# Kernel optimization log

Hardware: AMD Instinct MI355X
Metric: run time of the kernel (lower is better)

The kernel has to match this reference:

```python
import jax, jax.numpy as jnp
import numpy as np


def _relative_position_index(S):
    # Faithful to the torch buffer construction, computed once with numpy (static).
    coords = np.stack(np.meshgrid(np.arange(S), np.arange(S), indexing='ij'))  # (2,S,S)
    coords = coords.reshape(2, -1)                                             # (2,N)
    rel = coords[:, :, None] - coords[:, None, :]                              # (2,N,N)
    rel = rel.transpose(1, 2, 0).astype(np.int64)                              # (N,N,2)
    rel[:, :, 0] += S - 1
    rel[:, :, 1] += S - 1
    rel[:, :, 0] *= 2 * S - 1
    idx = rel.sum(-1)
    idx = idx[::-1, ::-1].copy()  # flipud(fliplr(...))
    return idx                    # (N,N) int64 in [0, (2S-1)^2)


def setup_inputs() -> dict:
    key = jax.random.key(0)
    ks = jax.random.split(key, 6)
    B, S, C, NH = 8, 32, 512, 16
    x = jax.random.normal(ks[0], (B, S, S, C), dtype=jnp.float32)
    qkv_w = jax.random.normal(ks[1], (3 * C, C), dtype=jnp.float32) * 0.02
    qkv_b = jax.random.normal(ks[2], (3 * C,), dtype=jnp.float32) * 0.02
    rpb = jax.random.normal(ks[3], (NH, 2 * S - 1, 2 * S - 1), dtype=jnp.float32) * 0.02
    proj_w = jax.random.normal(ks[4], (C, C), dtype=jnp.float32) * 0.02
    proj_b = jax.random.normal(ks[5], (C,), dtype=jnp.float32) * 0.02
    return {"x": x, "qkv_w": qkv_w, "qkv_b": qkv_b, "rpb": rpb,
            "proj_w": proj_w, "proj_b": proj_b}


def reference(x, qkv_w, qkv_b, rpb, proj_w, proj_b):
    B, H, W, C = x.shape
    N = H * W
    num_heads = rpb.shape[0]
    head_dim = C // num_heads
    scale = head_dim ** (-0.5)
    S = H

    idx = _relative_position_index(S)  # static numpy (N,N)

    qkv = x.reshape(B, N, C) @ qkv_w.T + qkv_b            # (B,N,3C)
    qkv = qkv.reshape(B, N, 3, num_heads, head_dim)
    qkv = jnp.transpose(qkv, (2, 0, 3, 1, 4))             # (3,B,h,N,d)
    q, k, v = qkv[0], qkv[1], qkv[2]

    attn = jnp.einsum('bhnd,bhmd->bhnm', q * scale, k)    # (B,h,N,N)
    # gather relative position bias: (h,(2S-1)^2)[:, idx] -> (h,N,N)
    bias = rpb.reshape(num_heads, -1)[:, idx]
    attn = jax.nn.softmax(attn + bias[None], axis=-1)

    out = jnp.einsum('bhnm,bhmd->bhnd', attn, v)          # (B,h,N,d)
    out = jnp.transpose(out, (0, 2, 1, 3)).reshape(B, H, W, C)
    return out @ proj_w.T + proj_b
```

## Files before the change

### kernel.cpp

```cpp
#include <hip/hip_runtime.h>

typedef __bf16 bf16x8 __attribute__((ext_vector_type(8)));
typedef float f32x4 __attribute__((ext_vector_type(4)));
typedef unsigned int u32x2 __attribute__((ext_vector_type(2)));
typedef unsigned short u16;
typedef unsigned int u32;

__device__ __forceinline__ float bf2f(u16 v) {
    union { unsigned u; float f; } x; x.u = ((unsigned)v) << 16; return x.f;
}
__device__ __forceinline__ u16 f2bf(float f) {
    union { float f; unsigned u; } x; x.f = f;
    unsigned r = x.u + 0x7fffu + ((x.u >> 16) & 1u);
    return (u16)(r >> 16);
}

__device__ __forceinline__ bool probe_is_f32(const void* xp) {
    const unsigned* p = (const unsigned*)xp;
    int hits = 0;
#pragma unroll
    for (int i = 0; i < 32; i++) {
        const unsigned e = (p[i] >> 7) & 0xffu;
        hits += (e >= 0x90u) ? 1 : 0;
    }
    return hits > 3;
}

__device__ __forceinline__ float ld1(const void* p, size_t i, bool isf32) {
    return isf32 ? ((const float*)p)[i] : bf2f(((const u16*)p)[i]);
}

__device__ __forceinline__ void gl2lds16(const void* g, void* l) {
    __builtin_amdgcn_global_load_lds(
        (const __attribute__((address_space(1))) u32*)g,
        (__attribute__((address_space(3))) u32*)l, 16, 0, 0);
}

__global__ __launch_bounds__(256)
void convert_inputs(const void* __restrict__ x, const void* __restrict__ qw,
                    const void* __restrict__ qb, const void* __restrict__ pw,
                    const void* __restrict__ pb, const void* __restrict__ rp,
                    u16* __restrict__ xbf, u16* __restrict__ qwbf,
                    u16* __restrict__ qbbf, u16* __restrict__ pwbf,
                    u16* __restrict__ pbbf, float* __restrict__ rpl2e)
{
    const bool isf32 = probe_is_f32(x);
    const int gid = blockIdx.x * 256 + threadIdx.x;
    const int gsz = gridDim.x * 256;

    struct Seg { const void* s; u16* d; int n; };
    const Seg segs[5] = {{x, xbf, 4194304}, {qw, qwbf, 786432}, {pw, pwbf, 262144},
                         {qb, qbbf, 1536}, {pb, pbbf, 512}};
    for (int t = 0; t < 5; t++) {
        const int n4 = segs[t].n >> 2;
        if (isf32) {
            const f32x4* s = (const f32x4*)segs[t].s;
            for (int i = gid; i < n4; i += gsz) {
                f32x4 v = s[i];
                ushort4 o;
                o.x = f2bf(v[0]); o.y = f2bf(v[1]); o.z = f2bf(v[2]); o.w = f2bf(v[3]);
                *(ushort4*)(segs[t].d + i * 4) = o;
            }
        } else {
            const ushort4* s = (const ushort4*)segs[t].s;
            for (int i = gid; i < n4; i += gsz) *(ushort4*)(segs[t].d + i * 4) = s[i];
        }
    }
    for (int i = gid; i < 63504; i += gsz)
        rpl2e[i] = ld1(rp, i, isf32) * 1.4426950408889634f;
}

template<int MODE, int BM>
__global__ __launch_bounds__(256, MODE == 1 ? 3 : 4)
void gemm_bt(const u16* __restrict__ A, const u16* __restrict__ W,
             const u16* __restrict__ bias, void* __restrict__ out,
             u16* __restrict__ q_out, u16* __restrict__ k_out, u16* __restrict__ v_out,
             const void* __restrict__ probe, int Nout, int K)
{
    __shared__ __align__(16) u16 As[2][BM * 32];
    __shared__ __align__(16) u16 Ws[2][128 * 32];
    constexpr int RW = BM / 32;

    const int tid  = threadIdx.x;
    const int lane = tid & 63;
    const int wave = tid >> 6;
    const int quad = lane >> 4;
    const int l16  = lane & 15;
    const int m0 = blockIdx.y * BM;
    const int n0 = blockIdx.x * 128;
    const int wm = (wave >> 1) * (BM / 2);
    const int wn = (wave & 1) * 64;

    f32x4 acc[RW][4] = {};

    for (int k0 = 0; k0 < K; k0 += 64) {
        __syncthreads();
        for (int u = 0; u < 2; u++) {
            {
                const u16* g = A + (size_t)(m0 + wave * 16 + (lane >> 2)) * K
                                 + k0 + u * 32 + (lane & 3) * 8;
                u16* l = As[u] + wave * 16 * 32;
                for (int p = 0; p < BM / 64; p++) gl2lds16(g + (size_t)p * 64 * K, l + p * 64 * 32);
            }
            {
                const u16* g = W + (size_t)(n0 + wave * 16 + (lane >> 2)) * K
                                 + k0 + u * 32 + (lane & 3) * 8;
                u16* l = Ws[u] + wave * 16 * 32;
                for (int p = 0; p < 2; p++) gl2lds16(g + (size_t)p * 64 * K, l + p * 64 * 32);
            }
        }
        __syncthreads();

        for (int u = 0; u < 2; u++) {
            bf16x8 af[RW], wf[4];
            for (int i = 0; i < RW; i++)
                af[i] = *(const bf16x8*)(As[u] + (wm + i * 16 + l16) * 32 + quad * 8);
            for (int j = 0; j < 4; j++)
                wf[j] = *(const bf16x8*)(Ws[u] + (wn + j * 16 + l16) * 32 + quad * 8);
            for (int i = 0; i < RW; i++)
                for (int j = 0; j < 4; j++)
                    acc[i][j] = __builtin_amdgcn_mfma_f32_16x16x32_bf16(af[i], wf[j], acc[i][j], 0, 0, 0);
        }
    }

    if (MODE == 0) {
        const bool isf32 = probe_is_f32(probe);
        for (int j = 0; j < 4; j++) {
            const int col = n0 + wn + j * 16 + l16;
            const float bv = bf2f(bias[col]);
            for (int i = 0; i < RW; i++) {
                const int rbase = m0 + wm + i * 16 + quad * 4;
                for (int r = 0; r < 4; r++) {
                    const float val = acc[i][j][r] + bv;
                    if (isf32) ((float*)out)[(size_t)(rbase + r) * Nout + col] = val;
                    else       ((u16*)out)[(size_t)(rbase + r) * Nout + col]  = f2bf(val);
                }
            }
        }
    } else {
        const int which = m0 >> 9;
        u16* dst = which == 0 ? q_out : (which == 1 ? k_out : v_out);
        float bv[RW][4];
        for (int i = 0; i < RW; i++) {
            const int row4 = m0 + wm + i * 16 + quad * 4;
            for (int r = 0; r < 4; r++) bv[i][r] = bf2f(bias[row4 + r]);
        }
        for (int j = 0; j < 4; j++) {
            const int tok = n0 + wn + j * 16 + l16;
            const int bi = tok >> 10, t = tok & 1023;
            for (int i = 0; i < RW; i++) {
                const int row4 = m0 + wm + i * 16 + quad * 4;
                const int h = (row4 >> 5) & 15;
                const int c = row4 & 31;
                ushort4 pk;
                pk.x = f2bf(acc[i][j][0] + bv[i][0]);
                pk.y = f2bf(acc[i][j][1] + bv[i][1]);
                pk.z = f2bf(acc[i][j][2] + bv[i][2]);
                pk.w = f2bf(acc[i][j][3] + bv[i][3]);
                *(ushort4*)(dst + ((size_t)(bi * 16 + h) * 1024 + t) * 32 + c) = pk;
            }
        }
    }
}

__global__ __launch_bounds__(256, 4)
void attn(const u16* __restrict__ q, const u16* __restrict__ k,
          const u16* __restrict__ v, const float* __restrict__ rpl2e,
          u16* __restrict__ o)
{
    __shared__ __align__(16) u16 Ks[2][64 * 40];
    __shared__ __align__(16) u16 Vt[2][32 * 72];
    __shared__ float biasT[63 * 37];

    const int tid  = threadIdx.x;
    const int lane = tid & 63;
    const int wave = tid >> 6;
    const int quad = lane >> 4;
    const int l16  = lane & 15;

    const int h  = blockIdx.x;
    const int qt = blockIdx.y;
    const int b  = blockIdx.z;
    const int n0 = qt * 128;
    const size_t base = ((size_t)(b * 16 + h)) * 32768;

    {
        const int row0 = 28 - 4 * qt;
        for (int idx = tid; idx < 2205; idx += 256) {
            const int rr = idx / 63, cc = idx % 63;
            biasT[cc * 37 + rr] =
                rpl2e[(size_t)h * 3969 + (size_t)(row0 + rr) * 63 + cc];
        }
    }
    const int vt_t = lane;
    const int vcg  = wave;
    uint4 kreg = *(const uint4*)(k + base + (size_t)(tid >> 2) * 32 + (tid & 3) * 8);
    uint4 vreg = *(const uint4*)(v + base + (size_t)vt_t * 32 + vcg * 8);
    *(uint4*)(Ks[0] + (tid >> 2) * 40 + (tid & 3) * 8) = kreg;
    {
        const u16* vr = (const u16*)&vreg;
#pragma unroll
        for (int jj = 0; jj < 8; jj++)
            Vt[0][(vcg * 8 + jj) * 72 + vt_t] = vr[jj];
    }

    bf16x8 qf[2];
    for (int g = 0; g < 2; g++) {
        union { uint4 u; bf16x8 f; } cv;
        cv.u = *(const uint4*)(q + base + (size_t)(n0 + g * 64 + wave * 16 + l16) * 32 + quad * 8);
        qf[g] = cv.f;
    }
    __syncthreads();

    bf16x8 ones;
    for (int i = 0; i < 8; i++) ones[i] = (__bf16)1.0f;

    f32x4 o_acc[2][3] = {};
    const int bn = (wave & 1) * 16 + l16;
    const int w2 = wave >> 1;
    const float SC = 0.25503485724582146f;

    const int cb = quad * 4 + 31 - bn;
    float X0[8], X1[8], Y0[8], Y1[8];
#pragma unroll
    for (int ci = 0; ci < 8; ci++) {
        const int c37 = (cb + (ci >> 2) * 16 + (ci & 3)) * 37;
        X0[ci] = biasT[c37 + (1 - w2)];
        X1[ci] = biasT[c37 + (2 - w2)];
        Y0[ci] = biasT[c37 + (3 - w2)];
        Y1[ci] = biasT[c37 + (4 - w2)];
    }

    for (int kt = 0; kt < 16; kt++) {
        const int cur = kt & 1;
        if (kt < 15) {
            const int mn = (kt + 1) * 64;
            kreg = *(const uint4*)(k + base + (size_t)(mn + (tid >> 2)) * 32 + (tid & 3) * 8);
            vreg = *(const uint4*)(v + base + (size_t)(mn + vt_t) * 32 + vcg * 8);
        }

        bf16x8 kf[4];
#pragma unroll
        for (int j = 0; j < 4; j++)
            kf[j] = *(const bf16x8*)(Ks[cur] + (j * 16 + l16) * 40 + quad * 8);
        bf16x8 vf[2][2];
#pragma unroll
        for (int kc = 0; kc < 2; kc++)
#pragma unroll
            for (int ct = 0; ct < 2; ct++)
                vf[kc][ct] = *(const bf16x8*)(Vt[cur] + (ct * 16 + l16) * 72 + kc * 32 + quad * 8);

#pragma unroll
        for (int g = 0; g < 2; g++) {
            f32x4 s4[4];
            const f32x4 zero = {};
#pragma unroll
            for (int j = 0; j < 4; j++)
                s4[j] = __builtin_amdgcn_mfma_f32_16x16x32_bf16(kf[j], qf[g], zero, 0, 0, 0);

            u32 Aw[4], Bw[4];
#pragma unroll
            for (int j = 0; j < 4; j++) {
                u16 pk[4];
#pragma unroll
                for (int r = 0; r < 4; r++) {
                    const int ci = (j & 1) * 4 + r;
                    const float bval = (j >> 1) ? (g ? X1[ci] : Y1[ci])
                                                : (g ? X0[ci] : Y0[ci]);
                    const float pv = __builtin_amdgcn_exp2f(s4[j][r] * SC + bval);
                    union { __bf16 b; u16 u; } cv; cv.b = (__bf16)pv;
                    pk[r] = cv.u;
                }
                Aw[j] = ((u32)pk[1] << 16) | pk[0];
                Bw[j] = ((u32)pk[3] << 16) | pk[2];
            }

#pragma unroll
            for (int kc = 0; kc < 2; kc++) {
                u32x2 ra = __builtin_amdgcn_permlane32_swap(Aw[2 * kc], Aw[2 * kc + 1], false, false);
                u32x2 wa = __builtin_amdgcn_permlane16_swap(ra.x, ra.y, false, false);
                u32x2 rb = __builtin_amdgcn_permlane32_swap(Bw[2 * kc], Bw[2 * kc + 1], false, false);
                u32x2 wb = __builtin_amdgcn_permlane16_swap(rb.x, rb.y, false, false);
                union { u32 w[4]; bf16x8 f; } pa;
                pa.w[0] = wa.x; pa.w[1] = wb.x; pa.w[2] = wa.y; pa.w[3] = wb.y;
#pragma unroll
                for (int ct = 0; ct < 2; ct++)
                    o_acc[g][ct] = __builtin_amdgcn_mfma_f32_16x16x32_bf16(pa.f, vf[kc][ct], o_acc[g][ct], 0, 0, 0);
                o_acc[g][2] = __builtin_amdgcn_mfma_f32_16x16x32_bf16(pa.f, ones, o_acc[g][2], 0, 0, 0);
            }
        }

        if (kt < 15) {
#pragma unroll
            for (int ci = 0; ci < 8; ci++) { X0[ci] = Y0[ci]; X1[ci] = Y1[ci]; }
            const int nr = 2 * kt - w2 + 5;
#pragma unroll
            for (int ci = 0; ci < 8; ci++) {
                const int c37 = (cb + (ci >> 2) * 16 + (ci & 3)) * 37;
                Y0[ci] = biasT[c37 + nr];
                Y1[ci] = biasT[c37 + nr + 1];
            }
            *(uint4*)(Ks[cur ^ 1] + (tid >> 2) * 40 + (tid & 3) * 8) = kreg;
            const u16* vr = (const u16*)&vreg;
#pragma unroll
            for (int jj = 0; jj < 8; jj++)
                Vt[cur ^ 1][(vcg * 8 + jj) * 72 + vt_t] = vr[jj];
        }
        __syncthreads();
    }

    for (int g = 0; g < 2; g++)
        for (int r = 0; r < 4; r++) {
            const float inv = __builtin_amdgcn_rcpf(o_acc[g][2][r]);
            const int n = n0 + g * 64 + wave * 16 + quad * 4 + r;
            u16* orow = o + ((size_t)b * 1024 + n) * 512 + h * 32;
            orow[l16]      = f2bf(o_acc[g][0][r] * inv);
            orow[16 + l16] = f2bf(o_acc[g][1][r] * inv);
        }
}

extern "C" void kernel_launch(void* const* d_in, const int* in_sizes, int n_in,
                              void* d_out, int out_size, void* d_ws, size_t ws_size,
                              hipStream_t stream) {
    const void* x      = d_in[0];
    const void* qkv_w  = d_in[1];
    const void* qkv_b  = d_in[2];
    const void* rpb    = d_in[3];
    const void* proj_w = d_in[4];
    const void* proj_b = d_in[5];

    u16* ws    = (u16*)d_ws;
    u16* kb    = ws;
    u16* vb    = ws + 4194304;
    u16* xbf   = ws + 8388608;
    u16* ao    = xbf;
    u16* qwbf  = ws + 12582912;
    u16* pwbf  = ws + 13369344;
    u16* qbbf  = ws + 13631488;
    u16* pbbf  = ws + 13633024;
    float* rpl2e = (float*)(ws + 13633536);
    u16* qb    = (u16*)d_out;

    convert_inputs<<<1024, 256, 0, stream>>>(x, qkv_w, qkv_b, proj_w, proj_b, rpb,
                                             xbf, qwbf, qbbf, pwbf, pbbf, rpl2e);

    dim3 g1(8192 / 128, 1536 / 128);
    gemm_bt<1, 128><<<g1, 256, 0, stream>>>(qwbf, xbf, qbbf, nullptr, qb, kb, vb, x, 8192, 512);

    dim3 g2(16, 8, 8);
    attn<<<g2, 256, 0, stream>>>(qb, kb, vb, rpl2e, ao);

    dim3 g3(512 / 128, 8192 / 64);
    gemm_bt<0, 64><<<g3, 256, 0, stream>>>(ao, pwbf, pbbf, d_out, nullptr, nullptr, nullptr, x, 512, 512);
}
```

Baseline: 149.0 us.

## Fuse x fp32-to-bf16 conversion into QKV GEMM load and fold scale/bias into MFMA

```diff
diff --git a/kernel.cpp b/kernel.cpp
--- a/kernel.cpp
+++ b/kernel.cpp
@@ -40,18 +40,18 @@
 void convert_inputs(const void* __restrict__ x, const void* __restrict__ qw,
                     const void* __restrict__ qb, const void* __restrict__ pw,
                     const void* __restrict__ pb, const void* __restrict__ rp,
-                    u16* __restrict__ xbf, u16* __restrict__ qwbf,
-                    u16* __restrict__ qbbf, u16* __restrict__ pwbf,
-                    u16* __restrict__ pbbf, float* __restrict__ rpl2e)
+                    u16* __restrict__ qwbf, u16* __restrict__ qbbf,
+                    u16* __restrict__ pwbf, u16* __restrict__ pbbf,
+                    float* __restrict__ rpl2e)
 {
     const bool isf32 = probe_is_f32(x);
     const int gid = blockIdx.x * 256 + threadIdx.x;
     const int gsz = gridDim.x * 256;
 
     struct Seg { const void* s; u16* d; int n; };
-    const Seg segs[5] = {{x, xbf, 4194304}, {qw, qwbf, 786432}, {pw, pwbf, 262144},
+    const Seg segs[4] = {{qw, qwbf, 786432}, {pw, pwbf, 262144},
                          {qb, qbbf, 1536}, {pb, pbbf, 512}};
-    for (int t = 0; t < 5; t++) {
+    for (int t = 0; t < 4; t++) {
         const int n4 = segs[t].n >> 2;
         if (isf32) {
             const f32x4* s = (const f32x4*)segs[t].s;
@@ -72,7 +72,7 @@
 
 template<int MODE, int BM>
 __global__ __launch_bounds__(256, MODE == 1 ? 3 : 4)
-void gemm_bt(const u16* __restrict__ A, const u16* __restrict__ W,
+void gemm_bt(const u16* __restrict__ A, const void* __restrict__ W,
              const u16* __restrict__ bias, void* __restrict__ out,
              u16* __restrict__ q_out, u16* __restrict__ k_out, u16* __restrict__ v_out,
              const void* __restrict__ probe, int Nout, int K)
@@ -91,6 +91,10 @@
     const int wm = (wave >> 1) * (BM / 2);
     const int wn = (wave & 1) * 64;
 
+    const bool isf32 = probe_is_f32(probe);
+    const u16* Wb = (const u16*)W;
+    const float* Wf = (const float*)W;
+
     f32x4 acc[RW][4] = {};
 
     for (int k0 = 0; k0 < K; k0 += 64) {
@@ -102,8 +106,21 @@
                 u16* l = As[u] + wave * 16 * 32;
                 for (int p = 0; p < BM / 64; p++) gl2lds16(g + (size_t)p * 64 * K, l + p * 64 * 32);
             }
-            {
-                const u16* g = W + (size_t)(n0 + wave * 16 + (lane >> 2)) * K
+            if (MODE == 1 && isf32) {
+                const float* gx = Wf + (size_t)(n0 + wave * 16 + (lane >> 2)) * K
+                                  + k0 + u * 32 + (lane & 3) * 8;
+                for (int p = 0; p < 2; p++) {
+                    f32x4 a = *(const f32x4*)(gx + (size_t)p * 64 * K);
+                    f32x4 c = *(const f32x4*)(gx + (size_t)p * 64 * K + 4);
+                    ushort4 lo, hi;
+                    lo.x = f2bf(a[0]); lo.y = f2bf(a[1]); lo.z = f2bf(a[2]); lo.w = f2bf(a[3]);
+                    hi.x = f2bf(c[0]); hi.y = f2bf(c[1]); hi.z = f2bf(c[2]); hi.w = f2bf(c[3]);
+                    u16* d = Ws[u] + wave * 16 * 32 + p * 64 * 32 + lane * 8;
+                    *(ushort4*)(d) = lo;
+                    *(ushort4*)(d + 4) = hi;
+                }
+            } else {
+                const u16* g = Wb + (size_t)(n0 + wave * 16 + (lane >> 2)) * K
                                  + k0 + u * 32 + (lane & 3) * 8;
                 u16* l = Ws[u] + wave * 16 * 32;
                 for (int p = 0; p < 2; p++) gl2lds16(g + (size_t)p * 64 * K, l + p * 64 * 32);
@@ -124,7 +141,6 @@
     }
 
     if (MODE == 0) {
-        const bool isf32 = probe_is_f32(probe);
         for (int j = 0; j < 4; j++) {
             const int col = n0 + wn + j * 16 + l16;
             const float bv = bf2f(bias[col]);
@@ -140,23 +156,24 @@
     } else {
         const int which = m0 >> 9;
         u16* dst = which == 0 ? q_out : (which == 1 ? k_out : v_out);
+        const float qsc = (which == 0) ? 0.25503485724582146f : 1.0f;
         float bv[RW][4];
         for (int i = 0; i < RW; i++) {
             const int row4 = m0 + wm + i * 16 + quad * 4;
-            for (int r = 0; r < 4; r++) bv[i][r] = bf2f(bias[row4 + r]);
+            for (int r = 0; r < 4; r++) bv[i][r] = bf2f(bias[row4 + r]) * qsc;
         }
         for (int j = 0; j < 4; j++) {
             const int tok = n0 + wn + j * 16 + l16;
             const int bi = tok >> 10, t = tok & 1023;
             for (int i = 0; i < RW; i++) {
+                ushort4 pk;
+                pk.x = f2bf(acc[i][j][0] * qsc + bv[i][0]);
+                pk.y = f2bf(acc[i][j][1] * qsc + bv[i][1]);
+                pk.z = f2bf(acc[i][j][2] * qsc + bv[i][2]);
+                pk.w = f2bf(acc[i][j][3] * qsc + bv[i][3]);
                 const int row4 = m0 + wm + i * 16 + quad * 4;
                 const int h = (row4 >> 5) & 15;
                 const int c = row4 & 31;
-                ushort4 pk;
-                pk.x = f2bf(acc[i][j][0] + bv[i][0]);
-                pk.y = f2bf(acc[i][j][1] + bv[i][1]);
-                pk.z = f2bf(acc[i][j][2] + bv[i][2]);
-                pk.w = f2bf(acc[i][j][3] + bv[i][3]);
                 *(ushort4*)(dst + ((size_t)(bi * 16 + h) * 1024 + t) * 32 + c) = pk;
             }
         }
@@ -218,18 +235,19 @@
     f32x4 o_acc[2][3] = {};
     const int bn = (wave & 1) * 16 + l16;
     const int w2 = wave >> 1;
-    const float SC = 0.25503485724582146f;
 
     const int cb = quad * 4 + 31 - bn;
-    float X0[8], X1[8], Y0[8], Y1[8];
-#pragma unroll
-    for (int ci = 0; ci < 8; ci++) {
-        const int c37 = (cb + (ci >> 2) * 16 + (ci & 3)) * 37;
-        X0[ci] = biasT[c37 + (1 - w2)];
-        X1[ci] = biasT[c37 + (2 - w2)];
-        Y0[ci] = biasT[c37 + (3 - w2)];
-        Y1[ci] = biasT[c37 + (4 - w2)];
-    }
+    f32x4 X0v[2], X1v[2], Y0v[2], Y1v[2];
+#pragma unroll
+    for (int p2 = 0; p2 < 2; p2++)
+#pragma unroll
+        for (int r = 0; r < 4; r++) {
+            const int c37 = (cb + p2 * 16 + r) * 37;
+            X0v[p2][r] = biasT[c37 + (1 - w2)];
+            X1v[p2][r] = biasT[c37 + (2 - w2)];
+            Y0v[p2][r] = biasT[c37 + (3 - w2)];
+            Y1v[p2][r] = biasT[c37 + (4 - w2)];
+        }
 
     for (int kt = 0; kt < 16; kt++) {
         const int cur = kt & 1;
@@ -253,10 +271,12 @@
 #pragma unroll
         for (int g = 0; g < 2; g++) {
             f32x4 s4[4];
-            const f32x4 zero = {};
-#pragma unroll
-            for (int j = 0; j < 4; j++)
-                s4[j] = __builtin_amdgcn_mfma_f32_16x16x32_bf16(kf[j], qf[g], zero, 0, 0, 0);
+#pragma unroll
+            for (int j = 0; j < 4; j++) {
+                const f32x4 Cb = g ? ((j >> 1) ? X1v[j & 1] : X0v[j & 1])
+                                   : ((j >> 1) ? Y1v[j & 1] : Y0v[j & 1]);
+                s4[j] = __builtin_amdgcn_mfma_f32_16x16x32_bf16(kf[j], qf[g], Cb, 0, 0, 0);
+            }
 
             u32 Aw[4], Bw[4];
 #pragma unroll
@@ -264,10 +284,7 @@
                 u16 pk[4];
 #pragma unroll
                 for (int r = 0; r < 4; r++) {
-                    const int ci = (j & 1) * 4 + r;
-                    const float bval = (j >> 1) ? (g ? X1[ci] : Y1[ci])
-                                                : (g ? X0[ci] : Y0[ci]);
-                    const float pv = __builtin_amdgcn_exp2f(s4[j][r] * SC + bval);
+                    const float pv = __builtin_amdgcn_exp2f(s4[j][r]);
                     union { __bf16 b; u16 u; } cv; cv.b = (__bf16)pv;
                     pk[r] = cv.u;
                 }
@@ -292,14 +309,16 @@
 
         if (kt < 15) {
 #pragma unroll
-            for (int ci = 0; ci < 8; ci++) { X0[ci] = Y0[ci]; X1[ci] = Y1[ci]; }
+            for (int p2 = 0; p2 < 2; p2++) { X0v[p2] = Y0v[p2]; X1v[p2] = Y1v[p2]; }
             const int nr = 2 * kt - w2 + 5;
 #pragma unroll
-            for (int ci = 0; ci < 8; ci++) {
-                const int c37 = (cb + (ci >> 2) * 16 + (ci & 3)) * 37;
-                Y0[ci] = biasT[c37 + nr];
-                Y1[ci] = biasT[c37 + nr + 1];
-            }
+            for (int p2 = 0; p2 < 2; p2++)
+#pragma unroll
+                for (int r = 0; r < 4; r++) {
+                    const int c37 = (cb + p2 * 16 + r) * 37;
+                    Y0v[p2][r] = biasT[c37 + nr];
+                    Y1v[p2][r] = biasT[c37 + nr + 1];
+                }
             *(uint4*)(Ks[cur ^ 1] + (tid >> 2) * 40 + (tid & 3) * 8) = kreg;
             const u16* vr = (const u16*)&vreg;
 #pragma unroll
@@ -332,8 +351,7 @@
     u16* ws    = (u16*)d_ws;
     u16* kb    = ws;
     u16* vb    = ws + 4194304;
-    u16* xbf   = ws + 8388608;
-    u16* ao    = xbf;
+    u16* ao    = ws + 8388608;
     u16* qwbf  = ws + 12582912;
     u16* pwbf  = ws + 13369344;
     u16* qbbf  = ws + 13631488;
@@ -341,11 +359,11 @@
     float* rpl2e = (float*)(ws + 13633536);
     u16* qb    = (u16*)d_out;
 
-    convert_inputs<<<1024, 256, 0, stream>>>(x, qkv_w, qkv_b, proj_w, proj_b, rpb,
-                                             xbf, qwbf, qbbf, pwbf, pbbf, rpl2e);
+    convert_inputs<<<256, 256, 0, stream>>>(x, qkv_w, qkv_b, proj_w, proj_b, rpb,
+                                            qwbf, qbbf, pwbf, pbbf, rpl2e);
 
     dim3 g1(8192 / 128, 1536 / 128);
-    gemm_bt<1, 128><<<g1, 256, 0, stream>>>(qwbf, xbf, qbbf, nullptr, qb, kb, vb, x, 8192, 512);
+    gemm_bt<1, 128><<<g1, 256, 0, stream>>>(qwbf, x, qbbf, nullptr, qb, kb, vb, x, 8192, 512);
 
     dim3 g2(16, 8, 8);
     attn<<<g2, 256, 0, stream>>>(qb, kb, vb, rpl2e, ao);
```

Result: no change. 151.4 us (+1.7%).
